# Optimization experiments

Hardware: AMD Instinct MI355X
Metric: run time of the kernel (lower is better)

The kernel has to match this reference:

```python
import jax, jax.numpy as jnp
import numpy as np

N_NODES = 20000
N_EDGES = 640000
NODE_DIM = 128
HIDDEN = 128
NUM_LAYERS = 3


def setup_inputs() -> dict:
    key = jax.random.key(0)
    ks = jax.random.split(key, 6)
    x = jax.random.normal(ks[0], (N_NODES, NODE_DIM), dtype=jnp.float32)
    edge_index = jax.random.randint(ks[1], (2, N_EDGES), 0, N_NODES, dtype=jnp.int64)
    s = 1.0 / np.sqrt(NODE_DIM)
    W_in = jax.random.uniform(ks[2], (NODE_DIM, HIDDEN), jnp.float32, -s, s)
    b_in = jax.random.uniform(ks[3], (HIDDEN,), jnp.float32, -s, s)
    sh = 1.0 / np.sqrt(HIDDEN)
    Ws = jax.random.uniform(ks[4], (NUM_LAYERS, HIDDEN, HIDDEN), jnp.float32, -sh, sh)
    bs = jax.random.uniform(ks[5], (NUM_LAYERS, HIDDEN), jnp.float32, -sh, sh)
    return {"x": x, "edge_index": edge_index, "W_in": W_in, "b_in": b_in, "Ws": Ws, "bs": bs}


def reference(x, edge_index, W_in, b_in, Ws, bs):
    N = x.shape[0]
    loop = jnp.arange(N, dtype=edge_index.dtype)
    src = jnp.concatenate([edge_index[0], loop])  # self-loops added (PyG GCNConv default)
    dst = jnp.concatenate([edge_index[1], loop])
    # symmetric normalization: deg computed on destination nodes
    deg = jax.ops.segment_sum(jnp.ones_like(dst, dtype=x.dtype), dst, num_segments=N)
    dis = jax.lax.rsqrt(jnp.where(deg > 0, deg, 1.0))
    norm = dis[src] * dis[dst]  # [E+N]
    h = x @ W_in + b_in
    for i in range(Ws.shape[0]):
        xw = h @ Ws[i]                              # [N, H]
        msg = xw[src] * norm[:, None]               # gather + scale
        agg = jax.ops.segment_sum(msg, dst, num_segments=N) + bs[i]
        h = jax.nn.relu(agg)                        # dropout p=0 -> identity
    return h
```

## Files before the change

### kernel.cpp

```cpp
#include <hip/hip_runtime.h>
#include <hip/hip_bf16.h>


#define HDIM 128

typedef __attribute__((ext_vector_type(8))) short s8v;
typedef __attribute__((ext_vector_type(4))) float f4v;

__device__ __forceinline__ ushort f2bf(float f) {
    uint u = __float_as_uint(f);
    u += 0x7FFFu + ((u >> 16) & 1u);
    return (ushort)(u >> 16);
}
__device__ __forceinline__ float bf2f(ushort h) {
    return __uint_as_float(((uint)h) << 16);
}


__global__ __launch_bounds__(256) void k_count(const int* __restrict__ dst,
                                               int* __restrict__ off4,
                                               int* __restrict__ rank, int E4) {
    int t = blockIdx.x * 256 + threadIdx.x;
    if (t >= E4) return;
    int4 d = ((const int4*)dst)[t];
    int4 r;
    r.x = atomicAdd(&off4[d.x * 4 + 0], 1);
    r.y = atomicAdd(&off4[d.y * 4 + 1], 1);
    r.z = atomicAdd(&off4[d.z * 4 + 2], 1);
    r.w = atomicAdd(&off4[d.w * 4 + 3], 1);
    ((int4*)rank)[t] = r;
}

__global__ __launch_bounds__(256) void k_scan_blk(int* __restrict__ off4,
                                                  float* __restrict__ dis,
                                                  int* __restrict__ bsum, int N) {
    int t = threadIdx.x;
    int total = N * 4;
    int base = blockIdx.x * 1024 + t * 4;
    int4 d = make_int4(0, 0, 0, 0);
    if (base < total) {
        d = *(const int4*)(off4 + base);
        dis[base >> 2] = rsqrtf((float)(d.x + d.y + d.z + d.w + 1));
    }
    int tsum = d.x + d.y + d.z + d.w;
    int lane = t & 63;
    int incl = tsum;
    #pragma unroll
    for (int ofs = 1; ofs < 64; ofs <<= 1) {
        int u = __shfl_up(incl, ofs);
        if (lane >= ofs) incl += u;
    }
    __shared__ int wsum[4];
    if (lane == 63) wsum[t >> 6] = incl;
    __syncthreads();
    int w = t >> 6;
    int woff = 0;
    for (int i = 0; i < w; ++i) woff += wsum[i];

    int run = woff + incl - tsum;
    if (base < total) {
        off4[base + 0] = run; run += d.x;
        off4[base + 1] = run; run += d.y;
        off4[base + 2] = run; run += d.z;
        off4[base + 3] = run;
    }
    if (t == 255) bsum[blockIdx.x] = woff + incl;
}

__global__ __launch_bounds__(256) void k_scan_add(int* __restrict__ off4,
                                                  const int* __restrict__ bsum,
                                                  int N, int E) {
    int bid = blockIdx.x;
    if (bid == 0) {
        if (threadIdx.x == 0) off4[N * 4] = E;
        return;
    }
    int p = 0;
    for (int i = 0; i < bid; ++i) p += bsum[i];
    int base = bid * 1024 + threadIdx.x * 4;
    if (base < N * 4) {
        int4 v = *(const int4*)(off4 + base);
        v.x += p; v.y += p; v.z += p; v.w += p;
        *(int4*)(off4 + base) = v;
    }
}

__global__ __launch_bounds__(256) void k_fill(const int* __restrict__ src,
                                              const int* __restrict__ dst,
                                              const int* __restrict__ off4,
                                              const int* __restrict__ rank,
                                              int* __restrict__ csr, int E4) {
    int t = blockIdx.x * 256 + threadIdx.x;
    if (t >= E4) return;
    int4 s = ((const int4*)src)[t];
    int4 d = ((const int4*)dst)[t];
    int4 r = ((const int4*)rank)[t];
    csr[off4[d.x * 4 + 0] + r.x] = s.x;
    csr[off4[d.y * 4 + 1] + r.y] = s.y;
    csr[off4[d.z * 4 + 2] + r.z] = s.z;
    csr[off4[d.w * 4 + 3] + r.w] = s.w;
}

__global__ __launch_bounds__(256) void k_pre(const float* __restrict__ W_in,
                                             const float* __restrict__ Ws,
                                             ushort* __restrict__ Wf,
                                             const float* __restrict__ x,
                                             ushort* __restrict__ hh,
                                             ushort* __restrict__ hl,
                                             int* __restrict__ off4,
                                             int N, int nbZ, int total4) {
    int bid = blockIdx.x;
    if (bid < nbZ) {
        int i = bid * 256 + threadIdx.x;
        if (i < N * 4) off4[i] = 0;
    } else if (bid < nbZ + 256) {
        int idx = (bid - nbZ) * 256 + threadIdx.x;
        int m = idx >> 14;
        int e = idx & 16383;
        int k = e >> 7, col = e & 127;
        const float* srcm = (m == 0) ? W_in : (Ws + (m - 1) * 16384);
        float w = srcm[k * 128 + col];
        ushort hi = f2bf(w);
        ushort lo = f2bf(w - bf2f(hi));
        int ks = k >> 5, lk = (k >> 3) & 3, j = k & 7;
        int ct = col >> 4, lane = lk * 16 + (col & 15);
        int o = m * 32768 + (ks * 8 + ct) * 512 + lane * 8 + j;
        Wf[o] = hi;
        Wf[o + 16384] = lo;
    } else {
        int i = (bid - nbZ - 256) * 256 + threadIdx.x;
        if (i >= total4) return;
        float4 v = ((const float4*)x)[i];
        ushort a0 = f2bf(v.x), a1 = f2bf(v.y), a2 = f2bf(v.z), a3 = f2bf(v.w);
        uint2 ph, pl;
        ph.x = (uint)a0 | ((uint)a1 << 16);
        ph.y = (uint)a2 | ((uint)a3 << 16);
        pl.x = (uint)f2bf(v.x - bf2f(a0)) | ((uint)f2bf(v.y - bf2f(a1)) << 16);
        pl.y = (uint)f2bf(v.z - bf2f(a2)) | ((uint)f2bf(v.w - bf2f(a3)) << 16);
        ((uint2*)hh)[i] = ph;
        ((uint2*)hl)[i] = pl;
    }
}

template<int MODE>
__global__ __launch_bounds__(256) void k_mgemm(const ushort* Ahi, const ushort* Alo,
                                               const ushort* __restrict__ Wf,
                                               const float* __restrict__ bias,
                                               const float* __restrict__ scale,
                                               ushort* xwb, ushort* outhi,
                                               ushort* outlo, int M) {
    int l = threadIdx.x & 63;
    int gw = blockIdx.x * 4 + (threadIdx.x >> 6);
    int strip = gw >> 1, ch = gw & 1;
    int r0 = strip * 16;
    int lr = l & 15, lk = l >> 4;
    int ar = r0 + lr; if (ar >= M) ar = M - 1;

    s8v ah0 = *(const s8v*)(Ahi + (long long)ar * HDIM + lk * 8);
    s8v ah1 = *(const s8v*)(Ahi + (long long)ar * HDIM + lk * 8 + 32);
    s8v ah2 = *(const s8v*)(Ahi + (long long)ar * HDIM + lk * 8 + 64);
    s8v ah3 = *(const s8v*)(Ahi + (long long)ar * HDIM + lk * 8 + 96);
    s8v al0 = *(const s8v*)(Alo + (long long)ar * HDIM + lk * 8);
    s8v al1 = *(const s8v*)(Alo + (long long)ar * HDIM + lk * 8 + 32);
    s8v al2 = *(const s8v*)(Alo + (long long)ar * HDIM + lk * 8 + 64);
    s8v al3 = *(const s8v*)(Alo + (long long)ar * HDIM + lk * 8 + 96);
    __syncthreads();

    f4v acc[4];
    #pragma unroll
    for (int c = 0; c < 4; ++c) acc[c] = (f4v){0.f, 0.f, 0.f, 0.f};

#define KSTEP(AH, AL, ksi)                                                          \
    {                                                                               \
        const ushort* wb = Wf + ((ksi) * 8 + ch * 4) * 512 + l * 8;                 \
        _Pragma("unroll")                                                           \
        for (int c = 0; c < 4; ++c) {                                               \
            s8v bh = *(const s8v*)(wb + c * 512);                                   \
            s8v bl = *(const s8v*)(wb + 16384 + c * 512);                           \
            acc[c] = __builtin_amdgcn_mfma_f32_16x16x32_bf16(AH, bh, acc[c], 0,0,0);\
            acc[c] = __builtin_amdgcn_mfma_f32_16x16x32_bf16(AH, bl, acc[c], 0,0,0);\
            acc[c] = __builtin_amdgcn_mfma_f32_16x16x32_bf16(AL, bh, acc[c], 0,0,0);\
        }                                                                           \
    }
    KSTEP(ah0, al0, 0)
    KSTEP(ah1, al1, 1)
    KSTEP(ah2, al2, 2)
    KSTEP(ah3, al3, 3)
#undef KSTEP

    if (r0 >= M) return;
    float bbv[4], sc[4];
    #pragma unroll
    for (int c = 0; c < 4; ++c) bbv[c] = bias ? bias[(ch * 4 + c) * 16 + lr] : 0.f;
    #pragma unroll
    for (int j = 0; j < 4; ++j) sc[j] = scale ? scale[r0 + lk * 4 + j] : 1.f;

    #pragma unroll
    for (int c = 0; c < 4; ++c) {
        #pragma unroll
        for (int j = 0; j < 4; ++j) {
            int row = r0 + lk * 4 + j;
            if (row >= M) continue;
            float o = (acc[c][j] + bbv[c]) * sc[j];
            if (MODE) {
                int col = (ch * 4 + c) * 16 + lr;
                ushort h = f2bf(o);
                outhi[(long long)row * HDIM + col] = h;
                outlo[(long long)row * HDIM + col] = f2bf(o - bf2f(h));
            } else {
                int cc = c * 16 + lr;
                xwb[((long long)ch * M + row) * 64 + cc] = f2bf(o);
            }
        }
    }
}

template<int LAST>
__global__ __launch_bounds__(256) void k_agg(const int* __restrict__ off4,
                                             const int* __restrict__ csr,
                                             const float* __restrict__ dis,
                                             const ushort* __restrict__ xwb,
                                             const float* __restrict__ b,
                                             float* __restrict__ outf,
                                             ushort* __restrict__ outhi,
                                             ushort* __restrict__ outlo, int N) {
    int lane = threadIdx.x & 63;
    int wv = threadIdx.x >> 6;
    int t = lane & 15, q = lane >> 4;
    int sl = blockIdx.x & 1;
    const ushort* xs = xwb + (long long)sl * N * 64;
    int v0 = (blockIdx.x >> 1) * 4 + wv;
    int vstride = (gridDim.x >> 1) * 4;

    float4 bb = ((const float4*)(b + sl * 64))[t];

#define GATH(sidx)                                                          \
    {                                                                       \
        uint2 u = *(const uint2*)(xs + (long long)(sidx) * 64 + (t << 2));  \
        ax += bf2f((ushort)u.x); ay += bf2f((ushort)(u.x >> 16));           \
        az += bf2f((ushort)u.y); aw += bf2f((ushort)(u.y >> 16));           \
    }
#define SEL(c) (q == 0 ? (c).x : q == 1 ? (c).y : q == 2 ? (c).z : (c).w)

    for (int v = v0; v < N; v += vstride) {
        int start = off4[v << 2];
        int end   = off4[(v << 2) + 4];
        float dv = dis[v];

        float ax = 0.f, ay = 0.f, az = 0.f, aw = 0.f;
        if (q == 0) GATH(v);

        int i = start;
        for (; i + 32 <= end; i += 32) {
            int ib = __builtin_amdgcn_readfirstlane(i);
            int4 c0 = *(const int4*)(csr + ib);
            int4 c1 = *(const int4*)(csr + ib + 4);
            int4 c2 = *(const int4*)(csr + ib + 8);
            int4 c3 = *(const int4*)(csr + ib + 12);
            int4 c4 = *(const int4*)(csr + ib + 16);
            int4 c5 = *(const int4*)(csr + ib + 20);
            int4 c6 = *(const int4*)(csr + ib + 24);
            int4 c7 = *(const int4*)(csr + ib + 28);
            int s0 = SEL(c0), s1 = SEL(c1), s2 = SEL(c2), s3 = SEL(c3);
            int s4 = SEL(c4), s5 = SEL(c5), s6 = SEL(c6), s7 = SEL(c7);
            GATH(s0); GATH(s1); GATH(s2); GATH(s3);
            GATH(s4); GATH(s5); GATH(s6); GATH(s7);
        }
        if (i + 16 <= end) {
            int ib = __builtin_amdgcn_readfirstlane(i);
            int4 c0 = *(const int4*)(csr + ib);
            int4 c1 = *(const int4*)(csr + ib + 4);
            int4 c2 = *(const int4*)(csr + ib + 8);
            int4 c3 = *(const int4*)(csr + ib + 12);
            int s0 = SEL(c0), s1 = SEL(c1), s2 = SEL(c2), s3 = SEL(c3);
            GATH(s0); GATH(s1); GATH(s2); GATH(s3);
            i += 16;
        }
        if (i + 8 <= end) {
            int ib = __builtin_amdgcn_readfirstlane(i);
            int4 c0 = *(const int4*)(csr + ib);
            int4 c1 = *(const int4*)(csr + ib + 4);
            int s0 = SEL(c0), s1 = SEL(c1);
            GATH(s0); GATH(s1);
            i += 8;
        }
        if (i + 4 <= end) {
            int ib = __builtin_amdgcn_readfirstlane(i);
            int4 c0 = *(const int4*)(csr + ib);
            int s0 = SEL(c0);
            GATH(s0);
            i += 4;
        }
        {
            int r = end - i;
            if (q < r) {
                int s = csr[__builtin_amdgcn_readfirstlane(i) + q];
                GATH(s);
            }
        }

        ax += __shfl_xor(ax, 16); ax += __shfl_xor(ax, 32);
        ay += __shfl_xor(ay, 16); ay += __shfl_xor(ay, 32);
        az += __shfl_xor(az, 16); az += __shfl_xor(az, 32);
        aw += __shfl_xor(aw, 16); aw += __shfl_xor(aw, 32);

        if (q == 0) {
            float ox = fmaxf(fmaf(dv, ax, bb.x), 0.f);
            float oy = fmaxf(fmaf(dv, ay, bb.y), 0.f);
            float oz = fmaxf(fmaf(dv, az, bb.z), 0.f);
            float ow = fmaxf(fmaf(dv, aw, bb.w), 0.f);
            long long oidx = (long long)v * HDIM + sl * 64 + (t << 2);
            if (LAST) {
                *(float4*)(outf + oidx) = make_float4(ox, oy, oz, ow);
            } else {
                ushort h0 = f2bf(ox), h1 = f2bf(oy), h2 = f2bf(oz), h3 = f2bf(ow);
                uint2 ph, pl;
                ph.x = (uint)h0 | ((uint)h1 << 16);
                ph.y = (uint)h2 | ((uint)h3 << 16);
                pl.x = (uint)f2bf(ox - bf2f(h0)) | ((uint)f2bf(oy - bf2f(h1)) << 16);
                pl.y = (uint)f2bf(oz - bf2f(h2)) | ((uint)f2bf(ow - bf2f(h3)) << 16);
                *(uint2*)(outhi + oidx) = ph;
                *(uint2*)(outlo + oidx) = pl;
            }
        }
    }
#undef GATH
#undef SEL
}

extern "C" void kernel_launch(void* const* d_in, const int* in_sizes, int n_in,
                              void* d_out, int out_size, void* d_ws, size_t ws_size,
                              hipStream_t stream) {
    const float* x    = (const float*)d_in[0];
    const int*   ei   = (const int*)d_in[1];
    const float* W_in = (const float*)d_in[2];
    const float* b_in = (const float*)d_in[3];
    const float* Ws   = (const float*)d_in[4];
    const float* bs   = (const float*)d_in[5];

    const int N = in_sizes[0] / HDIM;
    const int E = in_sizes[1] / 2;
    const int* src = ei;
    const int* dst = ei + E;

    float*  dis  = (float*)d_ws;
    int*    off4 = (int*)(dis + N);
    int*    csr  = off4 + 4 * N + 4;
    int*    rank = csr + E;
    ushort* hh   = (ushort*)(rank + E);
    ushort* hl   = hh + (long long)N * HDIM;
    ushort* xwb  = hl + (long long)N * HDIM;
    ushort* Wf   = (ushort*)d_out;

    int nbZ     = (4 * N + 255) / 256;
    int nb_E4   = (E / 4 + 255) / 256;
    int nb_scan = (4 * N + 1023) / 1024;
    int nwaves  = ((N + 15) / 16) * 2;
    int nb_mg   = (nwaves + 3) / 4;
    int total4  = N * (HDIM / 4);
    int nb_x4   = (total4 + 255) / 256;
    int nb_pre  = nbZ + 256 + nb_x4;
    int nb_agg  = 2048;

    k_pre<<<nb_pre, 256, 0, stream>>>(W_in, Ws, Wf, x, hh, hl, off4, N, nbZ, total4);

    k_count   <<<nb_E4,   256, 0, stream>>>(dst, off4, rank, E / 4);
    k_scan_blk<<<nb_scan, 256, 0, stream>>>(off4, dis, csr, N);
    k_scan_add<<<nb_scan, 256, 0, stream>>>(off4, csr, N, E);
    k_fill    <<<nb_E4,   256, 0, stream>>>(src, dst, off4, rank, csr, E / 4);

    k_mgemm<1><<<nb_mg, 256, 0, stream>>>(hh, hl, Wf, b_in, nullptr,
                                          nullptr, hh, hl, N);

    for (int layer = 0; layer < 3; ++layer) {
        const ushort* Wfm = Wf + (long long)(layer + 1) * 32768;
        const float* b = bs + (long long)layer * HDIM;
        k_mgemm<0><<<nb_mg, 256, 0, stream>>>(hh, hl, Wfm, nullptr, dis,
                                              xwb, nullptr, nullptr, N);
        if (layer == 2)
            k_agg<1><<<nb_agg, 256, 0, stream>>>(off4, csr, dis, xwb, b,
                                                 (float*)d_out, nullptr, nullptr, N);
        else
            k_agg<0><<<nb_agg, 256, 0, stream>>>(off4, csr, dis, xwb, b,
                                                 nullptr, hh, hl, N);
    }
}
```

Measured before the change: 169.3 us.

## Fold input projection into first layer weights and prefetch xw into cache

Precomputes W_in·Ws[0] and b_in·Ws[0] in the setup kernel, so the separate input-projection GEMM launch and its hi/lo write-back of h are removed. The GEMM grid is remapped so each block handles one column half, and an unneeded block barrier is dropped. Each aggregation kernel now begins by streaming its slice of xw through a dummy reduction to warm the cache before the irregular gathers. This folding changes the rounding of the fused weight compared with applying the two matrices in sequence, and the prefetch adds extra reads.

```diff
diff --git a/kernel.cpp b/kernel.cpp
--- a/kernel.cpp
+++ b/kernel.cpp
@@ -103,7 +103,9 @@
 
 __global__ __launch_bounds__(256) void k_pre(const float* __restrict__ W_in,
                                              const float* __restrict__ Ws,
+                                             const float* __restrict__ b_in,
                                              ushort* __restrict__ Wf,
+                                             float* __restrict__ bc,
                                              const float* __restrict__ x,
                                              ushort* __restrict__ hh,
                                              ushort* __restrict__ hl,
@@ -113,13 +115,20 @@
     if (bid < nbZ) {
         int i = bid * 256 + threadIdx.x;
         if (i < N * 4) off4[i] = 0;
-    } else if (bid < nbZ + 256) {
+    } else if (bid < nbZ + 192) {
         int idx = (bid - nbZ) * 256 + threadIdx.x;
         int m = idx >> 14;
         int e = idx & 16383;
         int k = e >> 7, col = e & 127;
-        const float* srcm = (m == 0) ? W_in : (Ws + (m - 1) * 16384);
-        float w = srcm[k * 128 + col];
+        float w;
+        if (m == 0) {
+            w = 0.f;
+            #pragma unroll 8
+            for (int j = 0; j < 128; ++j)
+                w = fmaf(W_in[k * 128 + j], Ws[j * 128 + col], w);
+        } else {
+            w = Ws[m * 16384 + k * 128 + col];
+        }
         ushort hi = f2bf(w);
         ushort lo = f2bf(w - bf2f(hi));
         int ks = k >> 5, lk = (k >> 3) & 3, j = k & 7;
@@ -127,8 +136,17 @@
         int o = m * 32768 + (ks * 8 + ct) * 512 + lane * 8 + j;
         Wf[o] = hi;
         Wf[o + 16384] = lo;
+    } else if (bid == nbZ + 192) {
+        int col = threadIdx.x;
+        if (col < 128) {
+            float v = 0.f;
+            #pragma unroll 8
+            for (int j = 0; j < 128; ++j)
+                v = fmaf(b_in[j], Ws[j * 128 + col], v);
+            bc[col] = v;
+        }
     } else {
-        int i = (bid - nbZ - 256) * 256 + threadIdx.x;
+        int i = (bid - nbZ - 193) * 256 + threadIdx.x;
         if (i >= total4) return;
         float4 v = ((const float4*)x)[i];
         ushort a0 = f2bf(v.x), a1 = f2bf(v.y), a2 = f2bf(v.z), a3 = f2bf(v.w);
@@ -142,16 +160,14 @@
     }
 }
 
-template<int MODE>
 __global__ __launch_bounds__(256) void k_mgemm(const ushort* Ahi, const ushort* Alo,
                                                const ushort* __restrict__ Wf,
                                                const float* __restrict__ bias,
                                                const float* __restrict__ scale,
-                                               ushort* xwb, ushort* outhi,
-                                               ushort* outlo, int M) {
+                                               ushort* xwb, int M) {
     int l = threadIdx.x & 63;
-    int gw = blockIdx.x * 4 + (threadIdx.x >> 6);
-    int strip = gw >> 1, ch = gw & 1;
+    int ch = blockIdx.x & 1;
+    int strip = (blockIdx.x >> 1) * 4 + (threadIdx.x >> 6);
     int r0 = strip * 16;
     int lr = l & 15, lk = l >> 4;
     int ar = r0 + lr; if (ar >= M) ar = M - 1;
@@ -164,7 +180,6 @@
     s8v al1 = *(const s8v*)(Alo + (long long)ar * HDIM + lk * 8 + 32);
     s8v al2 = *(const s8v*)(Alo + (long long)ar * HDIM + lk * 8 + 64);
     s8v al3 = *(const s8v*)(Alo + (long long)ar * HDIM + lk * 8 + 96);
-    __syncthreads();
 
     f4v acc[4];
     #pragma unroll
@@ -193,7 +208,7 @@
     #pragma unroll
     for (int c = 0; c < 4; ++c) bbv[c] = bias ? bias[(ch * 4 + c) * 16 + lr] : 0.f;
     #pragma unroll
-    for (int j = 0; j < 4; ++j) sc[j] = scale ? scale[r0 + lk * 4 + j] : 1.f;
+    for (int j = 0; j < 4; ++j) sc[j] = scale[r0 + lk * 4 + j];
 
     #pragma unroll
     for (int c = 0; c < 4; ++c) {
@@ -202,15 +217,8 @@
             int row = r0 + lk * 4 + j;
             if (row >= M) continue;
             float o = (acc[c][j] + bbv[c]) * sc[j];
-            if (MODE) {
-                int col = (ch * 4 + c) * 16 + lr;
-                ushort h = f2bf(o);
-                outhi[(long long)row * HDIM + col] = h;
-                outlo[(long long)row * HDIM + col] = f2bf(o - bf2f(h));
-            } else {
-                int cc = c * 16 + lr;
-                xwb[((long long)ch * M + row) * 64 + cc] = f2bf(o);
-            }
+            int cc = c * 16 + lr;
+            xwb[((long long)ch * M + row) * 64 + cc] = f2bf(o);
         }
     }
 }
@@ -229,6 +237,22 @@
     int t = lane & 15, q = lane >> 4;
     int sl = blockIdx.x & 1;
     const ushort* xs = xwb + (long long)sl * N * 64;
+
+    {
+        int lb = blockIdx.x >> 3;
+        const float4* p4 = (const float4*)xs;
+        int tot = N * 8;
+        int chunk = (tot + 255) >> 8;
+        int lo = lb * chunk;
+        int hi = lo + chunk; if (hi > tot) hi = tot;
+        float acc = 0.f;
+        for (int i = lo + (int)threadIdx.x; i < hi; i += 256) {
+            float4 u = p4[i];
+            acc += (u.x + u.y) + (u.z + u.w);
+        }
+        asm volatile("" :: "v"(acc));
+    }
+
     int v0 = (blockIdx.x >> 1) * 4 + wv;
     int vstride = (gridDim.x >> 1) * 4;
 
@@ -350,38 +374,40 @@
     ushort* hh   = (ushort*)(rank + E);
     ushort* hl   = hh + (long long)N * HDIM;
     ushort* xwb  = hl + (long long)N * HDIM;
+    float*  bc   = (float*)(xwb + (long long)2 * N * 64);
     ushort* Wf   = (ushort*)d_out;
 
     int nbZ     = (4 * N + 255) / 256;
     int nb_E4   = (E / 4 + 255) / 256;
     int nb_scan = (4 * N + 1023) / 1024;
-    int nwaves  = ((N + 15) / 16) * 2;
-    int nb_mg   = (nwaves + 3) / 4;
+    int strips  = (N + 15) / 16;
+    int nb_mg   = 2 * ((strips + 3) / 4);
     int total4  = N * (HDIM / 4);
     int nb_x4   = (total4 + 255) / 256;
-    int nb_pre  = nbZ + 256 + nb_x4;
+    int nb_pre  = nbZ + 192 + 1 + nb_x4;
     int nb_agg  = 2048;
 
-    k_pre<<<nb_pre, 256, 0, stream>>>(W_in, Ws, Wf, x, hh, hl, off4, N, nbZ, total4);
+    k_pre<<<nb_pre, 256, 0, stream>>>(W_in, Ws, b_in, Wf, bc, x, hh, hl,
+                                      off4, N, nbZ, total4);
 
     k_count   <<<nb_E4,   256, 0, stream>>>(dst, off4, rank, E / 4);
     k_scan_blk<<<nb_scan, 256, 0, stream>>>(off4, dis, csr, N);
     k_scan_add<<<nb_scan, 256, 0, stream>>>(off4, csr, N, E);
     k_fill    <<<nb_E4,   256, 0, stream>>>(src, dst, off4, rank, csr, E / 4);
 
-    k_mgemm<1><<<nb_mg, 256, 0, stream>>>(hh, hl, Wf, b_in, nullptr,
-                                          nullptr, hh, hl, N);
-
     for (int layer = 0; layer < 3; ++layer) {
-        const ushort* Wfm = Wf + (long long)(layer + 1) * 32768;
+        const ushort* Wfm = Wf + (long long)layer * 32768;
         const float* b = bs + (long long)layer * HDIM;
-        k_mgemm<0><<<nb_mg, 256, 0, stream>>>(hh, hl, Wfm, nullptr, dis,
-                                              xwb, nullptr, nullptr, N);
+        const ushort* Ah = (layer == 0) ? hh : hh;
+        k_mgemm<<<nb_mg, 256, 0, stream>>>(hh, hl, Wfm,
+                                           (layer == 0) ? bc : nullptr,
+                                           dis, xwb, N);
         if (layer == 2)
             k_agg<1><<<nb_agg, 256, 0, stream>>>(off4, csr, dis, xwb, b,
                                                  (float*)d_out, nullptr, nullptr, N);
         else
             k_agg<0><<<nb_agg, 256, 0, stream>>>(off4, csr, dis, xwb, b,
                                                  nullptr, hh, hl, N);
-    }
-}
+        (void)Ah;
+    }
+}
```

Measured after the change: 160.4 us. 1.06x faster.
